# Kernel optimization log

Measured on AMD Instinct MI355X. Metric: run time of the kernel, lower is better.

## Reference

```python
import jax, jax.numpy as jnp
import numpy as np

N, B, PG, L, HC, EC, H, NC, KNN = 256, 4, 64, 32, 128, 64, 4, 14, 8
D = HC // H
CUTOFF = 10.0
LOG2 = 0.6931471805599453

_counts = np.array([14, 5, 11, 8, 8, 6, 9, 9, 4, 10, 8, 8, 9, 8, 11, 7, 6, 7, 14, 12, 7])
RES_ATOM_MASK = (np.arange(14)[None, :] < _counts[:, None]).astype(np.float32)  # [21,14]


def _ln(x, g, b):
    mu = jnp.mean(x, -1, keepdims=True)
    var = jnp.mean((x - mu) ** 2, -1, keepdims=True)
    return (x - mu) / jnp.sqrt(var + 1e-5) * g + b


def _ssp(x):
    return jax.nn.softplus(x) - LOG2


def _safe_norm(x):
    return jnp.sqrt(jnp.maximum(jnp.sum(x * x, -1), 1e-12))


def _seg_softmax(x, idx, n):
    m = jax.ops.segment_max(x, idx, num_segments=n)
    e = jnp.exp(x - m[idx])
    s = jax.ops.segment_sum(e, idx, num_segments=n)
    return e / s[idx]


def _smear(d):
    offs = jnp.linspace(0.0, CUTOFF, EC)
    coeff = -0.5 / (offs[1] - offs[0]) ** 2
    return jnp.exp(coeff * (d[..., None] - offs) ** 2)


def _core(res_H, res_X, ligand_pos, ligand_feat, ligand_mask,
          ln_g, ln_b, ln1_g, ln1_b,
          WQ, WK, WV, WKl, WVl, WO, WOl, WOl1,
          Ti_w1, Ti_b1, Ti_w2, Ti_b2,
          sD_w1, sD_b1, sD_w2, sD_b2,
          sD1_w1, sD1_b1, sD1_w2, sD1_b2,
          res_S, batch, residue_mask, row1, col1):
    n = res_H.shape[0]
    bsz = ligand_feat.shape[0]
    lc = ligand_feat.shape[1]
    amask = jnp.asarray(RES_ATOM_MASK)[res_S]  # [n,14]

    # kNN graph on C-alpha (atom 1), per-graph, flow target_to_source, + self loops
    ctr = res_X[:, 1]
    d2 = jnp.sum((ctr[:, None] - ctr[None]) ** 2, -1)
    bad = (batch[:, None] != batch[None]) | jnp.eye(n, dtype=bool)
    _, nbr = jax.lax.top_k(-jnp.where(bad, jnp.inf, d2), KNN)
    row = jnp.concatenate([jnp.repeat(jnp.arange(n), KNN), jnp.arange(n)])
    col = jnp.concatenate([nbr.reshape(-1), jnp.arange(n)])

    Rij = _safe_norm(res_X[row][:, :, None] - res_X[col][:, None])  # [E,14,14]
    drep = _smear(Rij)  # [E,14,14,EC]

    res_Hn = _ln(res_H, ln_g, ln_b)
    Q = (res_Hn @ WQ.T).reshape(n, NC, H, D)
    Kt = (res_Hn @ WK.T).reshape(n, NC, H, D)
    V = (res_Hn @ WV.T).reshape(n, NC, H, D)

    logits = jnp.einsum('ephd,eqhd->ehpq', Q[row], Kt[col]) / np.sqrt(D)
    sig = jax.nn.relu(drep @ sD_w1.T + sD_b1) @ sD_w2.T + sD_b2  # [E,14,14,H]
    logits = logits + sig.transpose(0, 3, 1, 2)

    am_e = amask[row][:, :, None] * amask[col][:, None]  # [E,14,14]
    r = jnp.einsum('ep,ehpq,eq->eh', amask[row], logits, amask[col])
    r = r / jnp.sum(am_e, (-1, -2))[:, None]
    beta = _seg_softmax(r, row, n)  # [E,H]

    att = jax.nn.softmax(logits, -1) * am_e[:, None]
    att = att / (jnp.sum(jnp.abs(att), -1, keepdims=True) + 1e-7)
    aV = jnp.einsum('ehpq,eqhd->ehpd', att, V[col])
    updH = jax.ops.segment_sum(beta[:, :, None, None] * aV, row, num_segments=n)
    updH = updH.transpose(0, 2, 1, 3).reshape(n, NC, HC)
    res_H2 = (res_Hn + _ssp(updH) @ WO.T) * amask[..., None]

    Xij = res_X[row][:, :, None] - res_X[col][:, None]  # [E,14,14,3]
    Xij = Xij / (_safe_norm(Xij)[..., None] + 1e-5)
    Qf = Q.reshape(n, NC, HC)
    Kf = Kt.reshape(n, NC, HC)
    # T_i on concat([Q_p, K_q, dist]) computed as split matmuls (no big concat)
    hmid = (Qf[row] @ Ti_w1[:, :HC].T)[:, :, None, :] \
        + (Kf[col] @ Ti_w1[:, HC:2 * HC].T)[:, None, :, :] \
        + drep @ Ti_w1[:, 2 * HC:].T + Ti_b1  # [E,14,14,HC]
    f = (jax.nn.relu(hmid) @ Ti_w2.T + Ti_b2)[..., 0]  # [E,14,14]
    f = f * jnp.mean(att, 1)
    dX = jax.ops.segment_sum(jnp.mean(beta, -1)[:, None, None]
                             * jnp.sum(f[..., None] * Xij, -2), row, num_segments=n)
    res_X2 = jnp.where(residue_mask[:, None, None],
                       res_X + jnp.clip(dX, -3.0, 3.0), res_X)

    # residue <-> ligand cross attention over (editable residue, graph) edges
    lf = _ln(ligand_feat, ln1_g, ln1_b)
    Kl = (lf @ WKl.T).reshape(bsz, lc, H, D)
    Vl = (lf @ WVl.T).reshape(bsz, lc, H, D)
    Rij1 = _safe_norm(res_X2[row1][:, :, None] - ligand_pos[col1][:, None])
    drep1 = _smear(Rij1)  # [E1,14,L,EC]
    lg = jnp.einsum('ephd,eqhd->ehpq', Q[row1], Kl[col1]) / np.sqrt(D)
    sig1 = jax.nn.relu(drep1 @ sD1_w1.T + sD1_b1) @ sD1_w2.T + sD1_b2
    lg = lg + sig1.transpose(0, 3, 1, 2)

    am1 = amask[row1][:, :, None] * ligand_mask[col1][:, None]  # [E1,14,L]
    r1 = jnp.einsum('ep,ehpq,eq->eh', amask[row1], lg, ligand_mask[col1])
    r1 = r1 / jnp.sum(am1, (-1, -2))[:, None]
    beta1 = _seg_softmax(r1, col1, bsz)

    ar = jax.nn.softmax(lg, -1) * am1[:, None]
    ar = ar / (jnp.sum(jnp.abs(ar), -1, keepdims=True) + 1e-7)
    al = jax.nn.softmax(lg, -2) * am1[:, None]
    # faithful to source: lig branch divided by L1 norm of already-normalized ar
    al = al / (jnp.sum(jnp.abs(ar), -1, keepdims=True) + 1e-7)
    aVr = jnp.einsum('ehpq,eqhd->ehpd', ar, Vl[col1])  # [E1,H,14,D]
    e1 = row1.shape[0]
    res_H3 = res_H2.at[row1].add(
        _ssp(aVr.transpose(0, 2, 1, 3).reshape(e1, NC, HC)) @ WOl.T)
    res_H3 = res_H3 * amask[..., None]
    aVlg = jnp.einsum('ehpq,ephd->ehqd', al, V[row1])  # [E1,H,L,D]
    updL = jax.ops.segment_sum(beta1[:, :, None, None] * aVlg, col1, num_segments=bsz)
    lf2 = lf + _ssp(updL.transpose(0, 2, 1, 3).reshape(bsz, lc, HC)) @ WOl1.T
    return res_H3, res_X2, lf2


def setup_inputs() -> dict:
    key = jax.random.key(0)
    ks = jax.random.split(key, 40)
    rn = lambda i, shape, s=1.0: jax.random.normal(ks[i], shape, jnp.float32) * s
    w = lambda i, shape: jax.random.normal(ks[i], shape, jnp.float32) * 0.05
    res_H = rn(0, (N, NC, HC))
    res_X = rn(1, (N, NC, 3), 4.0)
    res_S = jax.random.randint(ks[2], (N,), 0, 21)
    batch = jnp.repeat(jnp.arange(B), PG)
    residue_mask = (jnp.arange(N) % PG) < 16
    row1 = jnp.asarray(np.nonzero(np.asarray(residue_mask))[0])
    col1 = row1 // PG
    ligand_pos = rn(3, (B, L, 3), 4.0)
    ligand_feat = rn(4, (B, L, HC))
    ligand_mask = jnp.tile((jnp.arange(L) < 24).astype(jnp.float32)[None], (B, 1))
    return dict(
        res_H=res_H, res_X=res_X, ligand_pos=ligand_pos, ligand_feat=ligand_feat,
        ligand_mask=ligand_mask,
        ln_g=jnp.ones((HC,)), ln_b=jnp.zeros((HC,)),
        ln1_g=jnp.ones((HC,)), ln1_b=jnp.zeros((HC,)),
        WQ=w(5, (HC, HC)), WK=w(6, (HC, HC)), WV=w(7, (HC, HC)),
        WKl=w(8, (HC, HC)), WVl=w(9, (HC, HC)),
        WO=w(10, (HC, HC)), WOl=w(11, (HC, HC)), WOl1=w(12, (HC, HC)),
        Ti_w1=w(13, (HC, 2 * HC + EC)), Ti_b1=jnp.zeros((HC,)),
        Ti_w2=w(14, (1, HC)), Ti_b2=jnp.zeros((1,)),
        sD_w1=w(15, (HC, EC)), sD_b1=jnp.zeros((HC,)),
        sD_w2=w(16, (H, HC)), sD_b2=jnp.zeros((H,)),
        sD1_w1=w(17, (HC, EC)), sD1_b1=jnp.zeros((HC,)),
        sD1_w2=w(18, (H, HC)), sD1_b2=jnp.zeros((H,)),
        res_S=res_S, batch=batch, residue_mask=residue_mask, row1=row1, col1=col1)


def reference(res_H, res_X, ligand_pos, ligand_feat, ligand_mask,
              ln_g, ln_b, ln1_g, ln1_b,
              WQ, WK, WV, WKl, WVl, WO, WOl, WOl1,
              Ti_w1, Ti_b1, Ti_w2, Ti_b2,
              sD_w1, sD_b1, sD_w2, sD_b2,
              sD1_w1, sD1_b1, sD1_w2, sD1_b2,
              res_S, batch, residue_mask, row1, col1):
    return _core(res_H, res_X, ligand_pos, ligand_feat, ligand_mask,
                 ln_g, ln_b, ln1_g, ln1_b,
                 WQ, WK, WV, WKl, WVl, WO, WOl, WOl1,
                 Ti_w1, Ti_b1, Ti_w2, Ti_b2,
                 sD_w1, sD_b1, sD_w2, sD_b2,
                 sD1_w1, sD1_b1, sD1_w2, sD1_b2,
                 res_S, batch, residue_mask, row1, col1)
```

## Files before the change

### kernel.cpp

```cpp
#include <hip/hip_runtime.h>
#include <hip/hip_bf16.h>
#include <math.h>

typedef __hip_bfloat16 bf16;

#define NRES 256
#define LC   32
#define HCH  128
#define ECH  64
#define NH   4
#define NCA  14
#define KNNK 8
#define DH   32
#define NKE  (NRES*KNNK)
#define NEDGE (NKE+NRES)
#define NE1  64
#define NROWS (NRES*NCA)

#define NT     3073
#define TSCALE 256.0f
#define DMAXT  12.0f

#define O_RESH   0
#define O_RESX   458752
#define O_LPOS   469504
#define O_LFEAT  469888
#define O_LMASK  486272
#define O_LNG    486400
#define O_LNB    486528
#define O_LN1G   486656
#define O_LN1B   486784
#define O_WQ     486912
#define O_WK     503296
#define O_WV     519680
#define O_WKL    536064
#define O_WVL    552448
#define O_WO     568832
#define O_WOL    585216
#define O_WOL1   601600
#define O_TIW1   617984
#define O_TIB1   658944
#define O_TIW2   659072
#define O_TIB2   659200
#define O_SDW1   659204
#define O_SDB1   667396
#define O_SDW2   667524
#define O_SDB2   668036
#define O_SD1W1  668040
#define O_SD1B1  676232
#define O_SD1W2  676360
#define O_SD1B2  676872
#define TOTCVT   676876
#define CVT_RSV  676880

#define OUTX_OFF 458752
#define OUTL_OFF 469504

__constant__ int c_counts[21] = {14,5,11,8,8,6,9,9,4,10,8,8,9,8,11,7,6,7,14,12,7};

__device__ __forceinline__ float b2f(bf16 x){ return __bfloat162float(x); }
__device__ __forceinline__ float sspf(float x){
  return fmaxf(x,0.f) + log1pf(expf(-fabsf(x))) - 0.6931471805599453f;
}
__device__ __forceinline__ float bflo(unsigned u){ return __uint_as_float(u<<16); }
__device__ __forceinline__ float bfhi(unsigned u){ return __uint_as_float(u & 0xffff0000u); }
__device__ __forceinline__ unsigned short f2bs(float v){ bf16 b=__float2bfloat16(v); return *(unsigned short*)&b; }
__device__ __forceinline__ unsigned pack2(float a, float b){
  return (unsigned)f2bs(a) | ((unsigned)f2bs(b)<<16);
}
__device__ __forceinline__ int ccount(int s){ return c_counts[s<0?0:(s>20?20:s)]; }
__device__ __forceinline__ void storeOut(void* out, int isbf, int idx, float v){
  if (isbf) ((bf16*)out)[idx] = __float2bfloat16(v);
  else      ((float*)out)[idx] = v;
}

__global__ __launch_bounds__(256) void kcvt(
    const void* s0,const void* s1,const void* s2,const void* s3,const void* s4,
    const void* s5,const void* s6,const void* s7,const void* s8,const void* s9,
    const void* s10,const void* s11,const void* s12,const void* s13,const void* s14,
    const void* s15,const void* s16,const void* s17,const void* s18,const void* s19,
    const void* s20,const void* s21,const void* s22,const void* s23,const void* s24,
    const void* s25,const void* s26,const void* s27,const void* s28,
    float* __restrict__ dst, int* __restrict__ flag)
{
  __shared__ int sflag;
  int tid = threadIdx.x;
  if (tid < 64){
    unsigned w = ((const unsigned*)s0)[tid];
    unsigned lo = w & 0xFFFFu;
    int ee = (lo >> 7) & 0xFF;
    int good = (lo == 0u) || (ee >= 121 && ee <= 133);
    unsigned long long m = __ballot(good);
    if (tid == 0){
      sflag = (__popcll(m) >= 40) ? 1 : 0;
      if (blockIdx.x == 0) flag[0] = sflag;
    }
  }
  __syncthreads();
  int isbf = sflag;
  int g = blockIdx.x*256 + tid;
  if (g >= TOTCVT) return;
  const void* src; int l;
  if      (g < O_RESX ) { src=s0;  l=g; }
  else if (g < O_LPOS ) { src=s1;  l=g-O_RESX; }
  else if (g < O_LFEAT) { src=s2;  l=g-O_LPOS; }
  else if (g < O_LMASK) { src=s3;  l=g-O_LFEAT; }
  else if (g < O_LNG  ) { src=s4;  l=g-O_LMASK; }
  else if (g < O_LNB  ) { src=s5;  l=g-O_LNG; }
  else if (g < O_LN1G ) { src=s6;  l=g-O_LNB; }
  else if (g < O_LN1B ) { src=s7;  l=g-O_LN1G; }
  else if (g < O_WQ   ) { src=s8;  l=g-O_LN1B; }
  else if (g < O_WK   ) { src=s9;  l=g-O_WQ; }
  else if (g < O_WV   ) { src=s10; l=g-O_WK; }
  else if (g < O_WKL  ) { src=s11; l=g-O_WV; }
  else if (g < O_WVL  ) { src=s12; l=g-O_WKL; }
  else if (g < O_WO   ) { src=s13; l=g-O_WVL; }
  else if (g < O_WOL  ) { src=s14; l=g-O_WO; }
  else if (g < O_WOL1 ) { src=s15; l=g-O_WOL; }
  else if (g < O_TIW1 ) { src=s16; l=g-O_WOL1; }
  else if (g < O_TIB1 ) { src=s17; l=g-O_TIW1; }
  else if (g < O_TIW2 ) { src=s18; l=g-O_TIB1; }
  else if (g < O_TIB2 ) { src=s19; l=g-O_TIW2; }
  else if (g < O_SDW1 ) { src=s20; l=0; }
  else if (g < O_SDB1 ) { src=s21; l=g-O_SDW1; }
  else if (g < O_SDW2 ) { src=s22; l=g-O_SDB1; }
  else if (g < O_SDB2 ) { src=s23; l=g-O_SDW2; }
  else if (g < O_SD1W1) { src=s24; l=g-O_SDB2; }
  else if (g < O_SD1B1) { src=s25; l=g-O_SD1W1; }
  else if (g < O_SD1W2) { src=s26; l=g-O_SD1B1; }
  else if (g < O_SD1B2) { src=s27; l=g-O_SD1W2; }
  else                  { src=s28; l=g-O_SD1B2; }
  float v = isbf ? b2f(((const bf16*)src)[l]) : ((const float*)src)[l];
  dst[g] = v;
}

__global__ __launch_bounds__(128) void kprep(const float* __restrict__ cvt, const int* __restrict__ row1,
    float* __restrict__ cT, float* __restrict__ sigT, float* __restrict__ sig1T,
    float* __restrict__ wt, int* __restrict__ inv_row)
{
  int b = blockIdx.x, o = threadIdx.x;
  if (b >= NT){
    int cb = b - NT;
    if (cb < 1280){
      int gid = cb*128 + o;
      int m = gid >> 14;
      int j = gid & 16383;
      int oo = j >> 7, c = j & 127;
      float v;
      switch(m){
        case 0: v = cvt[O_WQ  + j]; break;
        case 1: v = cvt[O_WK  + j]; break;
        case 2: v = cvt[O_WV  + j]; break;
        case 3: v = cvt[O_WO  + j]; break;
        case 4: v = cvt[O_WKL + j]; break;
        case 5: v = cvt[O_WVL + j]; break;
        case 6: v = cvt[O_WOL + j]; break;
        case 7: v = cvt[O_WOL1+ j]; break;
        case 8: v = cvt[O_TIW1 + oo*320 + c]; break;
        default:v = cvt[O_TIW1 + oo*320 + 128 + c]; break;
      }
      wt[m*16384 + c*128 + oo] = v;
    } else {
      for (int i=o;i<NRES;i+=128) inv_row[i] = -1;
      __syncthreads();
      if (o < NE1) inv_row[row1[o] & 255] = o;
    }
    return;
  }
  __shared__ float dr[64];
  __shared__ float W[128*65];
  __shared__ float h1[128], h1b[128];
  float d = (float)b * (1.0f/256.0f);
  const float step = 10.0f/63.0f;
  const float coef = -0.5f/(step*step);
  if (o < 64){ float t = d - step*(float)o; dr[o] = expf(coef*t*t); }
  for (int idx=o; idx<8192; idx+=128){ int oo=idx>>6, k=idx&63; W[oo*65+k] = cvt[O_TIW1 + oo*320 + 256 + k]; }
  __syncthreads();
  {
    float c = cvt[O_TIB1+o];
    for (int k=0;k<64;k++) c += dr[k]*W[o*65+k];
    cT[b*128+o] = c;
  }
  __syncthreads();
  for (int idx=o; idx<8192; idx+=128){ int oo=idx>>6, k=idx&63; W[oo*65+k] = cvt[O_SDW1 + idx]; }
  __syncthreads();
  {
    float a = cvt[O_SDB1+o];
    for (int k=0;k<64;k++) a += dr[k]*W[o*65+k];
    h1[o] = fmaxf(a,0.f);
  }
  __syncthreads();
  for (int idx=o; idx<8192; idx+=128){ int oo=idx>>6, k=idx&63; W[oo*65+k] = cvt[O_SD1W1 + idx]; }
  __syncthreads();
  {
    float a2 = cvt[O_SD1B1+o];
    for (int k=0;k<64;k++) a2 += dr[k]*W[o*65+k];
    h1b[o] = fmaxf(a2,0.f);
  }
  __syncthreads();
  if (o < 8){
    int h = o & 3;
    const float* hh = (o<4)? h1 : h1b;
    int wbase = (o<4)? O_SDW2 : O_SD1W2;
    int bbase = (o<4)? O_SDB2 : O_SD1B2;
    float s = cvt[bbase + h];
    for (int k=0;k<128;k++) s += hh[k]*cvt[wbase + h*128 + k];
    if (o<4) sigT[b*4+h] = s; else sig1T[b*4+h] = s;
  }
}

__global__ __launch_bounds__(256) void kProjAll(
    const float* __restrict__ cvt, const float* __restrict__ wt, const int* __restrict__ batch,
    float* __restrict__ resHn, bf16* __restrict__ Qw16, bf16* __restrict__ Kw16,
    bf16* __restrict__ Vw16, bf16* __restrict__ TQw16, bf16* __restrict__ TKw16,
    int* __restrict__ nbr, float* __restrict__ lf, bf16* __restrict__ Klw16, bf16* __restrict__ Vlw16)
{
  __shared__ float Xs[16*129];
  __shared__ float x2[2][HCH];
  __shared__ float sred2[2][2];
  int bb = blockIdx.x, tid = threadIdx.x;

  if (bb < 672){
    int m = bb / 224;
    int rt = (bb % 224) * 16;
    for (int i=tid; i<16*128; i+=256){
      int r=i>>7, c=i&127;
      Xs[r*129+c] = cvt[O_RESH + (rt+r)*HCH + c];
    }
    __syncthreads();
    {
      int wave = tid>>6, lane = tid&63;
      int r = wave*4 + (lane>>4);
      int cb = lane & 15;
      float s=0;
      #pragma unroll
      for (int j=0;j<8;j++) s += Xs[r*129 + cb + 16*j];
      #pragma unroll
      for (int off=1; off<16; off<<=1) s += __shfl_xor(s, off);
      float mu = s*(1.f/HCH);
      float q=0;
      #pragma unroll
      for (int j=0;j<8;j++){ float dv = Xs[r*129+cb+16*j]-mu; q += dv*dv; }
      #pragma unroll
      for (int off=1; off<16; off<<=1) q += __shfl_xor(q, off);
      float inv = rsqrtf(q*(1.f/HCH) + 1e-5f);
      #pragma unroll
      for (int j=0;j<8;j++){
        int c = cb + 16*j;
        float xh = (Xs[r*129+c]-mu)*inv*cvt[O_LNG+c] + cvt[O_LNB+c];
        Xs[r*129+c] = xh;
        if (m==0) resHn[(rt+r)*HCH+c] = xh;
      }
    }
    __syncthreads();
    int tc = (tid & 31) * 4;
    int tr = (tid >> 5) * 2;
    const float* W = wt + m*16384;
    float a00=0,a01=0,a02=0,a03=0, a10=0,a11=0,a12=0,a13=0;
    for (int c=0;c<HCH;c++){
      float4 w4 = *(const float4*)(W + c*128 + tc);
      float x0 = Xs[tr*129 + c];
      float x1 = Xs[(tr+1)*129 + c];
      a00 += x0*w4.x; a01 += x0*w4.y; a02 += x0*w4.z; a03 += x0*w4.w;
      a10 += x1*w4.x; a11 += x1*w4.y; a12 += x1*w4.z; a13 += x1*w4.w;
    }
    bf16* out = (m==0)? Qw16 : (m==1)? Kw16 : Vw16;
    {
      unsigned* o0 = (unsigned*)(out + (rt+tr  )*HCH + tc);
      unsigned* o1 = (unsigned*)(out + (rt+tr+1)*HCH + tc);
      o0[0]=pack2(a00,a01); o0[1]=pack2(a02,a03);
      o1[0]=pack2(a10,a11); o1[1]=pack2(a12,a13);
    }
    if (m == 2) return;
    __syncthreads();
    Xs[tr*129+tc]=a00; Xs[tr*129+tc+1]=a01; Xs[tr*129+tc+2]=a02; Xs[tr*129+tc+3]=a03;
    Xs[(tr+1)*129+tc]=a10; Xs[(tr+1)*129+tc+1]=a11; Xs[(tr+1)*129+tc+2]=a12; Xs[(tr+1)*129+tc+3]=a13;
    __syncthreads();
    const float* W2 = wt + (8+m)*16384;
    a00=0;a01=0;a02=0;a03=0; a10=0;a11=0;a12=0;a13=0;
    for (int c=0;c<HCH;c++){
      float4 w4 = *(const float4*)(W2 + c*128 + tc);
      float x0 = Xs[tr*129 + c];
      float x1 = Xs[(tr+1)*129 + c];
      a00 += x0*w4.x; a01 += x0*w4.y; a02 += x0*w4.z; a03 += x0*w4.w;
      a10 += x1*w4.x; a11 += x1*w4.y; a12 += x1*w4.z; a13 += x1*w4.w;
    }
    bf16* out2 = m ? TKw16 : TQw16;
    {
      unsigned* o0 = (unsigned*)(out2 + (rt+tr  )*HCH + tc);
      unsigned* o1 = (unsigned*)(out2 + (rt+tr+1)*HCH + tc);
      o0[0]=pack2(a00,a01); o0[1]=pack2(a02,a03);
      o1[0]=pack2(a10,a11); o1[1]=pack2(a12,a13);
    }
    return;
  }

  if (bb < 736){
    int wave = tid>>6, lane = tid&63;
    int n = (bb-672)*4 + wave;
    float cx = cvt[O_RESX+(n*NCA+1)*3+0];
    float cy = cvt[O_RESX+(n*NCA+1)*3+1];
    float cz = cvt[O_RESX+(n*NCA+1)*3+2];
    int bn = batch[n];
    float d2v[4]; int idv[4];
    #pragma unroll
    for (int t=0;t<4;t++){
      int j = lane + 64*t;
      float jx = cvt[O_RESX+(j*NCA+1)*3+0];
      float jy = cvt[O_RESX+(j*NCA+1)*3+1];
      float jz = cvt[O_RESX+(j*NCA+1)*3+2];
      float dx=cx-jx, dy=cy-jy, dz=cz-jz;
      float d2 = dx*dx+dy*dy+dz*dz;
      bool bad = (batch[j]!=bn) || (j==n);
      d2v[t] = bad ? INFINITY : d2;
      idv[t] = j;
    }
    for (int k=0;k<KNNK;k++){
      float dm = d2v[0]; int im = idv[0];
      #pragma unroll
      for (int t=1;t<4;t++)
        if (d2v[t]<dm || (d2v[t]==dm && idv[t]<im)){ dm=d2v[t]; im=idv[t]; }
      #pragma unroll
      for (int off=1; off<64; off<<=1){
        float dn = __shfl_xor(dm, off);
        int   in = __shfl_xor(im, off);
        if (dn<dm || (dn==dm && in<im)){ dm=dn; im=in; }
      }
      if (lane==0) nbr[n*KNNK+k] = im;
      #pragma unroll
      for (int t=0;t<4;t++) if (idv[t]==im) d2v[t] = INFINITY;
    }
    return;
  }

  int row = tid>>7, t = tid&127;
  int rb = (bb-736)*2 + row;
  float v = cvt[O_LFEAT + rb*HCH + t];
  float s=v;
  for (int off=1; off<64; off<<=1) s += __shfl_xor(s, off);
  if ((t&63)==0) sred2[row][t>>6]=s;
  __syncthreads();
  float mu=(sred2[row][0]+sred2[row][1])*(1.f/HCH);
  __syncthreads();
  float d=v-mu; s=d*d;
  for (int off=1; off<64; off<<=1) s += __shfl_xor(s, off);
  if ((t&63)==0) sred2[row][t>>6]=s;
  __syncthreads();
  float var=(sred2[row][0]+sred2[row][1])*(1.f/HCH);
  float xh = d*rsqrtf(var+1e-5f)*cvt[O_LN1G+t] + cvt[O_LN1B+t];
  x2[row][t]=xh; lf[rb*HCH+t]=xh;
  __syncthreads();
  const float* WKlt = wt + 4*16384;
  const float* WVlt = wt + 5*16384;
  float aK=0.f, aV=0.f;
  for (int c=0;c<HCH;c++){
    float xc=x2[row][c];
    aK += xc*WKlt[c*128+t];
    aV += xc*WVlt[c*128+t];
  }
  Klw16[rb*HCH+t]=__float2bfloat16(aK);
  Vlw16[rb*HCH+t]=__float2bfloat16(aV);
}

__global__ __launch_bounds__(256) void k3_edge(
    const float* __restrict__ cvt, const int* __restrict__ res_S, const int* __restrict__ nbr,
    const bf16* __restrict__ Qw16, const bf16* __restrict__ Kw16,
    const bf16* __restrict__ TQw16, const bf16* __restrict__ TKw16,
    const bf16* __restrict__ Vw16, const float* __restrict__ cT, const float* __restrict__ sigT,
    float* __restrict__ r_ws, bf16* __restrict__ aVe16, float* __restrict__ dXe)
{
  __shared__ unsigned Bq[14*66], Bk[14*66], Tq[14*66], Tk[14*66];
  __shared__ float LG[784], FR[196];
  __shared__ float tw2s[128], tb2s[1], Xr[42], Xc[42], amr[14], amc[14], rpart[56], cnts[2];
  unsigned* Vc = Tq;

  int b = blockIdx.x, tid = threadIdx.x;
  int rr = b & 255, slot = b >> 8;
  int e  = (slot < 8) ? (rr*8 + slot) : (2048 + rr);
  int cc = (slot < 8) ? (nbr[rr*8 + slot] & 255) : rr;

  const unsigned* Q32  = (const unsigned*)Qw16;
  const unsigned* K32  = (const unsigned*)Kw16;
  const unsigned* TQ32 = (const unsigned*)TQw16;
  const unsigned* TK32 = (const unsigned*)TKw16;
  const unsigned* V32  = (const unsigned*)Vw16;

  for (int i=tid;i<NCA*64;i+=256){
    int p=i>>6, k=i&63;
    Bq[p*66+k]=Q32[rr*896+i];  Bk[p*66+k]=K32[cc*896+i];
    Tq[p*66+k]=TQ32[rr*896+i]; Tk[p*66+k]=TK32[cc*896+i];
  }
  if (tid < 128) tw2s[tid]=cvt[O_TIW2+tid];
  if (tid == 128) tb2s[0]=cvt[O_TIB2];
  if (tid >= 136 && tid < 178){
    int i=tid-136; int p=i/3, jx=i%3;
    Xr[i] = cvt[O_RESX+(rr*NCA+p)*3+jx];
    Xc[i] = cvt[O_RESX+(cc*NCA+p)*3+jx];
  }
  if (tid >= 242 && tid < 242+NCA){
    int p=tid-242;
    amr[p] = (p < ccount(res_S[rr])) ? 1.f : 0.f;
    amc[p] = (p < ccount(res_S[cc])) ? 1.f : 0.f;
  }
  __syncthreads();

  if (tid < 196){
    int p = tid/14, q = tid%14;
    float dx=Xr[p*3]-Xc[q*3], dy=Xr[p*3+1]-Xc[q*3+1], dz=Xr[p*3+2]-Xc[q*3+2];
    float d = sqrtf(fmaxf(dx*dx+dy*dy+dz*dz, 1e-12f));
    int i0 = (int)(fminf(d, DMAXT)*TSCALE + 0.5f);
    float4 sg = ((const float4*)sigT)[i0];
    const float4* crow = (const float4*)(cT + i0*128);
    const uint2* Tq2 = (const uint2*)Tq;
    const uint2* Tk2 = (const uint2*)Tk;
    const uint2* Bq2 = (const uint2*)Bq;
    const uint2* Bk2 = (const uint2*)Bk;
    float fa = tb2s[0];
    #pragma unroll 8
    for (int j=0;j<32;j++){
      float4 cb = crow[j];
      uint2 ta = Tq2[p*33 + j];
      uint2 ka = Tk2[q*33 + j];
      int o = 4*j;
      fa += fmaxf(bflo(ta.x)+bflo(ka.x)+cb.x, 0.f)*tw2s[o  ];
      fa += fmaxf(bfhi(ta.x)+bfhi(ka.x)+cb.y, 0.f)*tw2s[o+1];
      fa += fmaxf(bflo(ta.y)+bflo(ka.y)+cb.z, 0.f)*tw2s[o+2];
      fa += fmaxf(bfhi(ta.y)+bfhi(ka.y)+cb.w, 0.f)*tw2s[o+3];
    }
    float qk0=0,qk1=0,qk2=0,qk3=0;
    #pragma unroll
    for (int j=0;j<8;j++){
      uint2 a0=Bq2[p*33+j],    b0=Bk2[q*33+j];
      uint2 a1=Bq2[p*33+8+j],  b1=Bk2[q*33+8+j];
      uint2 a2=Bq2[p*33+16+j], b2=Bk2[q*33+16+j];
      uint2 a3=Bq2[p*33+24+j], b3=Bk2[q*33+24+j];
      qk0 += bflo(a0.x)*bflo(b0.x) + bfhi(a0.x)*bfhi(b0.x) + bflo(a0.y)*bflo(b0.y) + bfhi(a0.y)*bfhi(b0.y);
      qk1 += bflo(a1.x)*bflo(b1.x) + bfhi(a1.x)*bfhi(b1.x) + bflo(a1.y)*bflo(b1.y) + bfhi(a1.y)*bfhi(b1.y);
      qk2 += bflo(a2.x)*bflo(b2.x) + bfhi(a2.x)*bfhi(b2.x) + bflo(a2.y)*bflo(b2.y) + bfhi(a2.y)*bfhi(b2.y);
      qk3 += bflo(a3.x)*bflo(b3.x) + bfhi(a3.x)*bfhi(b3.x) + bflo(a3.y)*bflo(b3.y) + bfhi(a3.y)*bfhi(b3.y);
    }
    const float isq = 0.17677669529663687f;
    LG[0*196+tid] = qk0*isq + sg.x;
    LG[1*196+tid] = qk1*isq + sg.y;
    LG[2*196+tid] = qk2*isq + sg.z;
    LG[3*196+tid] = qk3*isq + sg.w;
    FR[tid] = fa;
  }
  __syncthreads();

  for (int i=tid;i<NCA*64;i+=256){
    int p=i>>6, k=i&63;
    Vc[p*66+k]=V32[cc*896+i];
  }
  if (tid < 56){
    int h=tid/14, pp=tid%14;
    float ap = amr[pp];
    float row[NCA];
    float s=0;
    #pragma unroll
    for (int qq=0;qq<NCA;qq++){ row[qq]=LG[h*196+pp*14+qq]; s += row[qq]*amc[qq]; }
    rpart[h*14+pp] = s*ap;
    float m=-INFINITY;
    #pragma unroll
    for (int qq=0;qq<NCA;qq++) m=fmaxf(m,row[qq]);
    float sum=0;
    #pragma unroll
    for (int qq=0;qq<NCA;qq++){ row[qq]=expf(row[qq]-m); sum+=row[qq]; }
    float inv=1.f/sum, s2=0;
    #pragma unroll
    for (int qq=0;qq<NCA;qq++){ row[qq]=row[qq]*inv*ap*amc[qq]; s2+=row[qq]; }
    float inv2=1.f/(s2+1e-7f);
    #pragma unroll
    for (int qq=0;qq<NCA;qq++) LG[h*196+pp*14+qq]=row[qq]*inv2;
  }
  if (tid == 56){
    float sr=0, sc=0;
    for (int i=0;i<NCA;i++){ sr+=amr[i]; sc+=amc[i]; }
    cnts[0]=sr; cnts[1]=sc;
  }
  __syncthreads();
  if (tid < NH){
    float s=0;
    for (int pp=0;pp<NCA;pp++) s += rpart[tid*14+pp];
    r_ws[e*NH+tid] = s/(cnts[0]*cnts[1]);
  }
  if (tid < 196){
    int p=tid/14, q=tid%14;
    float ma = 0.25f*(LG[p*14+q] + LG[196+p*14+q] + LG[392+p*14+q] + LG[588+p*14+q]);
    FR[tid] *= ma;
  }
  __syncthreads();
  if (tid < NCA){
    int pp=tid;
    float ax=0, ay=0, az=0;
    #pragma unroll
    for (int qq=0;qq<NCA;qq++){
      float dx=Xr[pp*3]-Xc[qq*3], dy=Xr[pp*3+1]-Xc[qq*3+1], dz=Xr[pp*3+2]-Xc[qq*3+2];
      float nrm = sqrtf(fmaxf(dx*dx+dy*dy+dz*dz,1e-12f));
      float sc = FR[pp*14+qq]/(nrm+1e-5f);
      ax += sc*dx; ay += sc*dy; az += sc*dz;
    }
    dXe[(e*NCA+pp)*3+0]=ax; dXe[(e*NCA+pp)*3+1]=ay; dXe[(e*NCA+pp)*3+2]=az;
  }
  unsigned* aVe32 = (unsigned*)aVe16;
  #pragma unroll
  for (int rep=0;rep<4;rep++){
    int jdx = rep*256 + tid;
    if (jdx < 896){
      int h = jdx/224, rem = jdx%224;
      int pp = rem>>4, ddp = rem&15;
      float a0=0, a1=0;
      #pragma unroll
      for (int qq=0;qq<NCA;qq++){
        unsigned v = Vc[qq*66 + h*16 + ddp];
        float l = LG[h*196+pp*14+qq];
        a0 += l*bflo(v);
        a1 += l*bfhi(v);
      }
      aVe32[e*896 + jdx] = pack2(a0,a1);
    }
  }
}

__global__ __launch_bounds__(256) void k4_agg(
    const float* __restrict__ cvt, const int* __restrict__ res_S, const int* __restrict__ inv_row,
    const float* __restrict__ r_ws, const bf16* __restrict__ aVe16, const float* __restrict__ dXe,
    const float* __restrict__ resHn, const float* __restrict__ wt, const int* __restrict__ flag,
    float* __restrict__ resH2, float* __restrict__ resX2, void* __restrict__ d_out)
{
  int n = blockIdx.x, tid = threadIdx.x;
  __shared__ float beta[9][NH];
  __shared__ float betam[9];
  __shared__ float Xs[NCA][HCH];
  if (tid < NH){
    int h = tid;
    float rv[9], m=-INFINITY;
    #pragma unroll
    for (int k=0;k<9;k++){
      int ek = (k<KNNK)? n*KNNK+k : NKE+n;
      rv[k] = r_ws[ek*NH+h];
      m = fmaxf(m, rv[k]);
    }
    float s=0;
    #pragma unroll
    for (int k=0;k<9;k++){ rv[k]=expf(rv[k]-m); s+=rv[k]; }
    #pragma unroll
    for (int k=0;k<9;k++) beta[k][h]=rv[k]/s;
  }
  __syncthreads();
  if (tid < 9) betam[tid] = 0.25f*(beta[tid][0]+beta[tid][1]+beta[tid][2]+beta[tid][3]);
  int col = tid & 127, ph = tid >> 7;
  int h = col>>5, dd = col&31;
  float bh[9];
  #pragma unroll
  for (int k=0;k<9;k++) bh[k]=beta[k][h];
  #pragma unroll
  for (int i=0;i<7;i++){
    int p = ph + 2*i;
    float u=0;
    #pragma unroll
    for (int k=0;k<9;k++){
      int ek = (k<KNNK)? n*KNNK+k : NKE+n;
      u += bh[k]*b2f(aVe16[ek*1792 + h*448 + p*32 + dd]);
    }
    Xs[p][col] = sspf(u);
  }
  __syncthreads();
  const float* WOt = wt + 3*16384;
  float acc[7];
  #pragma unroll
  for (int i=0;i<7;i++) acc[i]=0.f;
  for (int c=0;c<HCH;c++){
    float w = WOt[c*128+col];
    #pragma unroll
    for (int i=0;i<7;i++) acc[i] += Xs[ph+2*i][c]*w;
  }
  int cnt = ccount(res_S[n]);
  #pragma unroll
  for (int i=0;i<7;i++){
    int p = ph + 2*i;
    float am = (p<cnt)?1.f:0.f;
    float outv = (resHn[(n*NCA+p)*HCH+col] + acc[i])*am;
    resH2[(n*NCA+p)*HCH+col] = outv;
  }
  if (tid < NCA*3){
    int isbf = *flag;
    int p=tid/3, jx=tid%3;
    float s=0;
    #pragma unroll
    for (int k=0;k<9;k++){
      int ek=(k<KNNK)? n*KNNK+k : NKE+n;
      s += betam[k]*dXe[(ek*NCA+p)*3+jx];
    }
    float base = cvt[O_RESX+(n*NCA+p)*3+jx];
    float v = (inv_row[n]>=0) ? base + fminf(fmaxf(s,-3.f),3.f) : base;
    resX2[(n*NCA+p)*3+jx] = v;
    storeOut(d_out, isbf, OUTX_OFF + (n*NCA+p)*3+jx, v);
  }
}

__global__ __launch_bounds__(256) void k6_lig(
    const float* __restrict__ cvt, const int* __restrict__ res_S,
    const int* __restrict__ row1, const int* __restrict__ col1,
    const float* __restrict__ resX2, const bf16* __restrict__ Qw16, const bf16* __restrict__ Klw16,
    const bf16* __restrict__ Vw16, const bf16* __restrict__ Vlw16, const float* __restrict__ sig1T,
    float* __restrict__ r1_ws, float* __restrict__ aVr, float* __restrict__ aVlg)
{
  __shared__ __align__(16) float S[10042];
  float* Bq  = S;
  float* Bk  = S + 1848;
  float* LG  = S;
  float* Vl  = S + 1848;
  float* ALs = S + 6104;
  float* Vr  = S + 7896;
  float* EX  = S + 9744;
  float* Xr = EX;
  float* Lp = EX + 42;
  float* amr = EX + 138;
  float* lm  = EX + 152;
  float* s2r = EX + 184;
  float* rpart = EX + 240;
  float* cnts  = EX + 296;
  int e = blockIdx.x, tid = threadIdx.x;
  int rr = row1[e] & 255, cb = col1[e] & 3;

  for (int i=tid;i<NCA*HCH;i+=256){ int p=i>>7,c=i&127; Bq[p*132+c]=b2f(Qw16[rr*1792+i]); Vr[p*132+c]=b2f(Vw16[rr*1792+i]); }
  for (int i=tid;i<LC*HCH;i+=256){ int q=i>>7,c=i&127; Bk[q*133+c]=b2f(Klw16[cb*LC*HCH+i]); }
  if (tid >= 8 && tid < 50){ int i=tid-8; int p=i/3,jx=i%3; Xr[i]=resX2[(rr*NCA+p)*3+jx]; }
  if (tid >= 64 && tid < 160){ int i=tid-64; int q=i/3,jx=i%3; Lp[i]=cvt[O_LPOS+(cb*LC+q)*3+jx]; }
  if (tid >= 160 && tid < 160+NCA) amr[tid-160]=((tid-160) < ccount(res_S[rr]))?1.f:0.f;
  if (tid >= 192 && tid < 224) lm[tid-192]=cvt[O_LMASK + cb*LC + tid-192];
  __syncthreads();

  float l0[2][4];
  int npair = (tid < 192) ? 2 : 1;
  for (int w=0; w<npair; w++){
    int pair = tid + w*256;
    int p = pair>>5, q = pair&31;
    float dx=Xr[p*3]-Lp[q*3], dy=Xr[p*3+1]-Lp[q*3+1], dz=Xr[p*3+2]-Lp[q*3+2];
    float d = sqrtf(fmaxf(dx*dx+dy*dy+dz*dz,1e-12f));
    int i0 = (int)(fminf(d, DMAXT)*TSCALE + 0.5f);
    float4 sg = ((const float4*)sig1T)[i0];
    float q0=0,q1=0,q2=0,q3=0;
    #pragma unroll
    for (int dd=0;dd<DH;dd++){
      q0 += Bq[p*132+dd]   *Bk[q*133+dd];
      q1 += Bq[p*132+32+dd]*Bk[q*133+32+dd];
      q2 += Bq[p*132+64+dd]*Bk[q*133+64+dd];
      q3 += Bq[p*132+96+dd]*Bk[q*133+96+dd];
    }
    const float isq=0.17677669529663687f;
    l0[w][0]=q0*isq+sg.x; l0[w][1]=q1*isq+sg.y; l0[w][2]=q2*isq+sg.z; l0[w][3]=q3*isq+sg.w;
  }
  __syncthreads();
  for (int w=0; w<npair; w++){
    int pair = tid + w*256;
    LG[0*448+pair]=l0[w][0]; LG[1*448+pair]=l0[w][1]; LG[2*448+pair]=l0[w][2]; LG[3*448+pair]=l0[w][3];
  }
  for (int i=tid;i<LC*HCH;i+=256){ int q=i>>7,c=i&127; Vl[q*132+c]=b2f(Vlw16[cb*LC*HCH+i]); }
  __syncthreads();

  if (tid < 56){
    int h=tid/14, pp=tid%14;
    float ap=amr[pp];
    float s=0, m=-INFINITY;
    for (int qq=0;qq<LC;qq++){ float v=LG[h*448+pp*32+qq]; s+=v*lm[qq]; m=fmaxf(m,v); }
    rpart[h*14+pp]=s*ap;
    float sum=0;
    for (int qq=0;qq<LC;qq++) sum+=expf(LG[h*448+pp*32+qq]-m);
    float inv=1.f/sum, s2=0;
    for (int qq=0;qq<LC;qq++) s2 += expf(LG[h*448+pp*32+qq]-m)*inv*ap*lm[qq];
    s2r[h*14+pp] = s2/(s2+1e-7f);
  }
  if (tid==56){
    float sr=0,sl=0;
    for(int i=0;i<NCA;i++) sr+=amr[i];
    for(int i=0;i<LC;i++) sl+=lm[i];
    cnts[0]=sr; cnts[1]=sl;
  }
  __syncthreads();
  if (tid < NH){
    float s=0; for (int pp=0;pp<NCA;pp++) s+=rpart[tid*14+pp];
    r1_ws[e*NH+tid]=s/(cnts[0]*cnts[1]);
  }
  if (tid < NH*LC){
    int h=tid>>5, qq=tid&31;
    float m=-INFINITY;
    for (int pp=0;pp<NCA;pp++) m=fmaxf(m,LG[h*448+pp*32+qq]);
    float sum=0;
    for (int pp=0;pp<NCA;pp++) sum+=expf(LG[h*448+pp*32+qq]-m);
    float inv=1.f/sum;
    float lq=lm[qq];
    for (int pp=0;pp<NCA;pp++){
      float a=expf(LG[h*448+pp*32+qq]-m)*inv*amr[pp]*lq;
      ALs[h*448+pp*32+qq]=a/(s2r[h*14+pp]+1e-7f);
    }
  }
  __syncthreads();
  if (tid < 56){
    int h=tid/14, pp=tid%14;
    float ap=amr[pp];
    float m=-INFINITY;
    for (int qq=0;qq<LC;qq++) m=fmaxf(m,LG[h*448+pp*32+qq]);
    float row[LC];
    float sum=0;
    for (int qq=0;qq<LC;qq++){ row[qq]=expf(LG[h*448+pp*32+qq]-m); sum+=row[qq]; }
    float inv=1.f/sum, s2=0;
    for (int qq=0;qq<LC;qq++){ row[qq]=row[qq]*inv*ap*lm[qq]; s2+=row[qq]; }
    float inv2=1.f/(s2+1e-7f);
    for (int qq=0;qq<LC;qq++) LG[h*448+pp*32+qq]=row[qq]*inv2;
  }
  __syncthreads();
  for (int j=tid;j<NH*NCA*DH;j+=256){
    int h=j/448, rem=j%448, pp=rem>>5, dd=rem&31;
    float acc=0;
    #pragma unroll
    for (int qq=0;qq<LC;qq++) acc += LG[h*448+pp*32+qq]*Vl[qq*132+h*32+dd];
    aVr[e*1792+j]=acc;
  }
  for (int j=tid;j<NH*LC*DH;j+=256){
    int h=j>>10, rem=j&1023, qq=rem>>5, dd=rem&31;
    float acc=0;
    #pragma unroll
    for (int pp=0;pp<NCA;pp++) acc += ALs[h*448+pp*32+qq]*Vr[pp*132+h*32+dd];
    aVlg[e*4096+j]=acc;
  }
}

__global__ __launch_bounds__(256) void k78_final(
    const int* __restrict__ inv_row, const int* __restrict__ res_S, const int* __restrict__ col1,
    const float* __restrict__ resH2, const float* __restrict__ aVr,
    const float* __restrict__ r1_ws, const float* __restrict__ aVlg, const float* __restrict__ lf,
    const float* __restrict__ wt, const int* __restrict__ flag, void* __restrict__ d_out)
{
  int bb = blockIdx.x, tid = threadIdx.x;
  if (bb < 256){
    int n = bb;
    int e = inv_row[n];
    __shared__ float G[NCA][HCH];
    if (e>=0){
      for (int j=tid;j<NCA*HCH;j+=256){
        int h=j/448, rem=j%448, pp=rem>>5, dd=rem&31;
        G[pp][h*DH+dd] = sspf(aVr[e*1792+j]);
      }
    }
    __syncthreads();
    int col = tid & 127, ph = tid >> 7;
    float acc[7];
    #pragma unroll
    for (int i=0;i<7;i++) acc[i]=0.f;
    if (e>=0){
      const float* WOlt = wt + 6*16384;
      for (int c=0;c<HCH;c++){
        float w=WOlt[c*128+col];
        #pragma unroll
        for (int i=0;i<7;i++) acc[i]+=G[ph+2*i][c]*w;
      }
    }
    int cnt=ccount(res_S[n]);
    int isbf = *flag;
    #pragma unroll
    for (int i=0;i<7;i++){
      int p = ph + 2*i;
      float am=(p<cnt)?1.f:0.f;
      float v=(resH2[(n*NCA+p)*HCH+col]+acc[i])*am;
      storeOut(d_out, isbf, (n*NCA+p)*HCH+col, v);
    }
    return;
  }
  int rb = bb - 256;
  int b = rb>>5, q = rb&31;
  __shared__ float bw[NE1][NH];
  __shared__ float xs[HCH];
  if (tid<NH){
    int h=tid;
    float m=-INFINITY;
    for (int e=0;e<NE1;e++) if ((col1[e]&3)==b) m=fmaxf(m, r1_ws[e*NH+h]);
    float s=0;
    for (int e=0;e<NE1;e++) if ((col1[e]&3)==b) s+=expf(r1_ws[e*NH+h]-m);
    for (int e=0;e<NE1;e++) bw[e][h] = ((col1[e]&3)==b)? expf(r1_ws[e*NH+h]-m)/s : 0.f;
  }
  __syncthreads();
  if (tid < 128){
    int h=tid>>5, dd=tid&31;
    float u=0;
    for (int e=0;e<NE1;e++) u += bw[e][h]*aVlg[e*4096 + h*1024 + q*32 + dd];
    xs[tid]=sspf(u);
  }
  __syncthreads();
  if (tid < 128){
    const float* WOl1t = wt + 7*16384;
    float acc=0;
    for (int c=0;c<HCH;c++) acc += xs[c]*WOl1t[c*128+tid];
    float v = lf[rb*HCH+tid] + acc;
    storeOut(d_out, *flag, OUTL_OFF + rb*HCH+tid, v);
  }
}

extern "C" void kernel_launch(void* const* d_in, const int* in_sizes, int n_in,
                              void* d_out, int out_size, void* d_ws, size_t ws_size,
                              hipStream_t stream)
{
  const int* res_S = (const int*)d_in[29];
  const int* batch = (const int*)d_in[30];
  const int* row1  = (const int*)d_in[32];
  const int* col1  = (const int*)d_in[33];

  float* wsf = (float*)d_ws;
  size_t o = 0;
  int*   flag    = (int*)(wsf + o); o += 4;
  float* cvt     = wsf + o; o += CVT_RSV;
  float* wt      = wsf + o; o += 10*16384;
  int*   inv_row = (int*)(wsf + o); o += 256;
  int*   nbr     = (int*)(wsf + o); o += NRES*KNNK;
  float* resHn   = wsf + o; o += NROWS*HCH;
  bf16*  Qw16    = (bf16*)(wsf + o); o += NROWS*HCH/2;
  bf16*  Kw16    = (bf16*)(wsf + o); o += NROWS*HCH/2;
  bf16*  Vw16    = (bf16*)(wsf + o); o += NROWS*HCH/2;
  bf16*  TQw16   = (bf16*)(wsf + o); o += NROWS*HCH/2;
  bf16*  TKw16   = (bf16*)(wsf + o); o += NROWS*HCH/2;
  float* r_ws    = wsf + o; o += NEDGE*NH;
  bf16*  aVe16   = (bf16*)(wsf + o); o += (size_t)NEDGE*1792/2;
  float* dXe     = wsf + o; o += NEDGE*NCA*3;
  float* resH2   = wsf + o; o += NROWS*HCH;
  float* resX2   = wsf + o; o += NRES*NCA*3;
  float* lf      = wsf + o; o += 4*LC*HCH;
  bf16*  Klw16   = (bf16*)(wsf + o); o += 4*LC*HCH/2;
  bf16*  Vlw16   = (bf16*)(wsf + o); o += 4*LC*HCH/2;
  float* r1w     = wsf + o; o += NE1*NH;
  float* aVrw    = wsf + o; o += NE1*1792;
  float* aVlgw   = wsf + o; o += NE1*4096;
  float* cT      = wsf + o; o += (size_t)NT*128;
  float* sigT    = wsf + o; o += NT*4;
  float* sig1T   = wsf + o; o += NT*4;

  kcvt<<<(TOTCVT+255)/256, 256, 0, stream>>>(
      d_in[0],d_in[1],d_in[2],d_in[3],d_in[4],d_in[5],d_in[6],d_in[7],d_in[8],
      d_in[9],d_in[10],d_in[11],d_in[12],d_in[13],d_in[14],d_in[15],d_in[16],
      d_in[17],d_in[18],d_in[19],d_in[20],d_in[21],d_in[22],d_in[23],d_in[24],
      d_in[25],d_in[26],d_in[27],d_in[28], cvt, flag);
  kprep<<<NT + 1280 + 1, 128, 0, stream>>>(cvt, row1, cT, sigT, sig1T, wt, inv_row);
  kProjAll<<<800, 256, 0, stream>>>(cvt, wt, batch, resHn, Qw16, Kw16, Vw16, TQw16, TKw16,
                                    nbr, lf, Klw16, Vlw16);
  k3_edge<<<NEDGE, 256, 0, stream>>>(cvt, res_S, nbr, Qw16, Kw16, TQw16, TKw16, Vw16, cT, sigT,
                                     r_ws, aVe16, dXe);
  k4_agg<<<NRES, 256, 0, stream>>>(cvt, res_S, inv_row, r_ws, aVe16, dXe, resHn, wt, flag,
                                   resH2, resX2, d_out);
  k6_lig<<<NE1, 256, 0, stream>>>(cvt, res_S, row1, col1, resX2, Qw16, Klw16, Vw16, Vlw16, sig1T,
                                  r1w, aVrw, aVlgw);
  k78_final<<<384, 256, 0, stream>>>(inv_row, res_S, col1, resH2, aVrw, r1w, aVlgw, lf,
                                     wt, flag, d_out);
}
```

Before: 279.3 us.

## Fuse weight transpose into convert kernel, batch table build, widen edge LDS loads

```diff
diff --git a/kernel.cpp b/kernel.cpp
--- a/kernel.cpp
+++ b/kernel.cpp
@@ -52,9 +52,12 @@
 #define O_SD1B2  676872
 #define TOTCVT   676876
 #define CVT_RSV  676880
+#define NCVTB    2645
 
 #define OUTX_OFF 458752
 #define OUTL_OFF 469504
+
+#define SR3 68
 
 __constant__ int c_counts[21] = {14,5,11,8,8,6,9,9,4,10,8,8,9,8,11,7,6,7,14,12,7};
 
@@ -81,10 +84,18 @@
     const void* s15,const void* s16,const void* s17,const void* s18,const void* s19,
     const void* s20,const void* s21,const void* s22,const void* s23,const void* s24,
     const void* s25,const void* s26,const void* s27,const void* s28,
-    float* __restrict__ dst, int* __restrict__ flag)
+    const int* __restrict__ row1,
+    float* __restrict__ dst, float* __restrict__ wt, int* __restrict__ inv_row,
+    int* __restrict__ flag)
 {
+  int tid = threadIdx.x;
+  if (blockIdx.x == NCVTB){
+    if (tid < NRES) inv_row[tid] = -1;
+    __syncthreads();
+    if (tid < NE1) inv_row[row1[tid] & 255] = tid;
+    return;
+  }
   __shared__ int sflag;
-  int tid = threadIdx.x;
   if (tid < 64){
     unsigned w = ((const unsigned*)s0)[tid];
     unsigned lo = w & 0xFFFFu;
@@ -132,80 +143,79 @@
   else                  { src=s28; l=g-O_SD1B2; }
   float v = isbf ? b2f(((const bf16*)src)[l]) : ((const float*)src)[l];
   dst[g] = v;
-}
-
-__global__ __launch_bounds__(128) void kprep(const float* __restrict__ cvt, const int* __restrict__ row1,
-    float* __restrict__ cT, float* __restrict__ sigT, float* __restrict__ sig1T,
-    float* __restrict__ wt, int* __restrict__ inv_row)
+  if (g >= O_WQ && g < O_TIW1){
+    int r = (g-O_WQ)>>14, j = (g-O_WQ)&16383;
+    int oo = j>>7, c = j&127;
+    int slot = (r==3)?4 : (r==4)?5 : (r==5)?3 : r;
+    wt[slot*16384 + c*128 + oo] = v;
+  } else if (g >= O_TIW1 && g < O_TIB1){
+    int ll = g - O_TIW1;
+    int oo = ll/320, c = ll - oo*320;
+    if (c < 128)      wt[8*16384 + c*128 + oo] = v;
+    else if (c < 256) wt[9*16384 + (c-128)*128 + oo] = v;
+  }
+}
+
+__global__ __launch_bounds__(128) void ktab(const float* __restrict__ cvt,
+    float* __restrict__ cT, float* __restrict__ sigT, float* __restrict__ sig1T)
 {
   int b = blockIdx.x, o = threadIdx.x;
-  if (b >= NT){
-    int cb = b - NT;
-    if (cb < 1280){
-      int gid = cb*128 + o;
-      int m = gid >> 14;
-      int j = gid & 16383;
-      int oo = j >> 7, c = j & 127;
-      float v;
-      switch(m){
-        case 0: v = cvt[O_WQ  + j]; break;
-        case 1: v = cvt[O_WK  + j]; break;
-        case 2: v = cvt[O_WV  + j]; break;
-        case 3: v = cvt[O_WO  + j]; break;
-        case 4: v = cvt[O_WKL + j]; break;
-        case 5: v = cvt[O_WVL + j]; break;
-        case 6: v = cvt[O_WOL + j]; break;
-        case 7: v = cvt[O_WOL1+ j]; break;
-        case 8: v = cvt[O_TIW1 + oo*320 + c]; break;
-        default:v = cvt[O_TIW1 + oo*320 + 128 + c]; break;
-      }
-      wt[m*16384 + c*128 + oo] = v;
-    } else {
-      for (int i=o;i<NRES;i+=128) inv_row[i] = -1;
-      __syncthreads();
-      if (o < NE1) inv_row[row1[o] & 255] = o;
-    }
-    return;
-  }
-  __shared__ float dr[64];
+  int i0 = b*16;
   __shared__ float W[128*65];
-  __shared__ float h1[128], h1b[128];
-  float d = (float)b * (1.0f/256.0f);
+  __shared__ float dr[16][65];
+  __shared__ float h1[16][130];
+  __shared__ float h1b[16][130];
   const float step = 10.0f/63.0f;
   const float coef = -0.5f/(step*step);
-  if (o < 64){ float t = d - step*(float)o; dr[o] = expf(coef*t*t); }
+  for (int idx=o; idx<16*64; idx+=128){
+    int i=idx>>6, k=idx&63;
+    float d = (float)(i0+i)*(1.0f/256.0f);
+    float t = d - step*(float)k;
+    dr[i][k] = expf(coef*t*t);
+  }
   for (int idx=o; idx<8192; idx+=128){ int oo=idx>>6, k=idx&63; W[oo*65+k] = cvt[O_TIW1 + oo*320 + 256 + k]; }
   __syncthreads();
   {
-    float c = cvt[O_TIB1+o];
-    for (int k=0;k<64;k++) c += dr[k]*W[o*65+k];
-    cT[b*128+o] = c;
+    float bias = cvt[O_TIB1+o];
+    for (int i=0;i<16 && i0+i<NT;i++){
+      float c = bias;
+      for (int k=0;k<64;k++) c += dr[i][k]*W[o*65+k];
+      cT[(i0+i)*128+o] = c;
+    }
   }
   __syncthreads();
   for (int idx=o; idx<8192; idx+=128){ int oo=idx>>6, k=idx&63; W[oo*65+k] = cvt[O_SDW1 + idx]; }
   __syncthreads();
   {
-    float a = cvt[O_SDB1+o];
-    for (int k=0;k<64;k++) a += dr[k]*W[o*65+k];
-    h1[o] = fmaxf(a,0.f);
+    float bias = cvt[O_SDB1+o];
+    for (int i=0;i<16;i++){
+      float a = bias;
+      for (int k=0;k<64;k++) a += dr[i][k]*W[o*65+k];
+      h1[i][o] = fmaxf(a,0.f);
+    }
   }
   __syncthreads();
   for (int idx=o; idx<8192; idx+=128){ int oo=idx>>6, k=idx&63; W[oo*65+k] = cvt[O_SD1W1 + idx]; }
   __syncthreads();
   {
-    float a2 = cvt[O_SD1B1+o];
-    for (int k=0;k<64;k++) a2 += dr[k]*W[o*65+k];
-    h1b[o] = fmaxf(a2,0.f);
-  }
-  __syncthreads();
-  if (o < 8){
-    int h = o & 3;
-    const float* hh = (o<4)? h1 : h1b;
-    int wbase = (o<4)? O_SDW2 : O_SD1W2;
-    int bbase = (o<4)? O_SDB2 : O_SD1B2;
-    float s = cvt[bbase + h];
-    for (int k=0;k<128;k++) s += hh[k]*cvt[wbase + h*128 + k];
-    if (o<4) sigT[b*4+h] = s; else sig1T[b*4+h] = s;
+    float bias = cvt[O_SD1B1+o];
+    for (int i=0;i<16;i++){
+      float a = bias;
+      for (int k=0;k<64;k++) a += dr[i][k]*W[o*65+k];
+      h1b[i][o] = fmaxf(a,0.f);
+    }
+  }
+  __syncthreads();
+  {
+    int i = o>>3, sub = o&7, h = sub&3, path = sub>>2;
+    if (i0+i < NT){
+      const float* hh = path ? h1b[i] : h1[i];
+      int wbase = path ? O_SD1W2 : O_SDW2;
+      int bbase = path ? O_SD1B2 : O_SDB2;
+      float s = cvt[bbase + h];
+      for (int k=0;k<128;k++) s += hh[k]*cvt[wbase + h*128 + k];
+      if (path) sig1T[(i0+i)*4+h] = s; else sigT[(i0+i)*4+h] = s;
+    }
   }
 }
 
@@ -369,7 +379,7 @@
     const bf16* __restrict__ Vw16, const float* __restrict__ cT, const float* __restrict__ sigT,
     float* __restrict__ r_ws, bf16* __restrict__ aVe16, float* __restrict__ dXe)
 {
-  __shared__ unsigned Bq[14*66], Bk[14*66], Tq[14*66], Tk[14*66];
+  __shared__ __align__(16) unsigned Bq[14*SR3], Bk[14*SR3], Tq[14*SR3], Tk[14*SR3];
   __shared__ float LG[784], FR[196];
   __shared__ float tw2s[128], tb2s[1], Xr[42], Xc[42], amr[14], amc[14], rpart[56], cnts[2];
   unsigned* Vc = Tq;
@@ -387,8 +397,8 @@
 
   for (int i=tid;i<NCA*64;i+=256){
     int p=i>>6, k=i&63;
-    Bq[p*66+k]=Q32[rr*896+i];  Bk[p*66+k]=K32[cc*896+i];
-    Tq[p*66+k]=TQ32[rr*896+i]; Tk[p*66+k]=TK32[cc*896+i];
+    Bq[p*SR3+k]=Q32[rr*896+i];  Bk[p*SR3+k]=K32[cc*896+i];
+    Tq[p*SR3+k]=TQ32[rr*896+i]; Tk[p*SR3+k]=TK32[cc*896+i];
   }
   if (tid < 128) tw2s[tid]=cvt[O_TIW2+tid];
   if (tid == 128) tb2s[0]=cvt[O_TIB2];
@@ -411,33 +421,41 @@
     int i0 = (int)(fminf(d, DMAXT)*TSCALE + 0.5f);
     float4 sg = ((const float4*)sigT)[i0];
     const float4* crow = (const float4*)(cT + i0*128);
-    const uint2* Tq2 = (const uint2*)Tq;
-    const uint2* Tk2 = (const uint2*)Tk;
-    const uint2* Bq2 = (const uint2*)Bq;
-    const uint2* Bk2 = (const uint2*)Bk;
+    const uint4* Tq4 = (const uint4*)Tq;
+    const uint4* Tk4 = (const uint4*)Tk;
+    const uint4* Bq4 = (const uint4*)Bq;
+    const uint4* Bk4 = (const uint4*)Bk;
     float fa = tb2s[0];
-    #pragma unroll 8
-    for (int j=0;j<32;j++){
-      float4 cb = crow[j];
-      uint2 ta = Tq2[p*33 + j];
-      uint2 ka = Tk2[q*33 + j];
-      int o = 4*j;
-      fa += fmaxf(bflo(ta.x)+bflo(ka.x)+cb.x, 0.f)*tw2s[o  ];
-      fa += fmaxf(bfhi(ta.x)+bfhi(ka.x)+cb.y, 0.f)*tw2s[o+1];
-      fa += fmaxf(bflo(ta.y)+bflo(ka.y)+cb.z, 0.f)*tw2s[o+2];
-      fa += fmaxf(bfhi(ta.y)+bfhi(ka.y)+cb.w, 0.f)*tw2s[o+3];
+    #pragma unroll 4
+    for (int j=0;j<16;j++){
+      uint4 ta = Tq4[p*17 + j];
+      uint4 ka = Tk4[q*17 + j];
+      float4 cb0 = crow[2*j], cb1 = crow[2*j+1];
+      int o = 8*j;
+      fa += fmaxf(bflo(ta.x)+bflo(ka.x)+cb0.x, 0.f)*tw2s[o  ];
+      fa += fmaxf(bfhi(ta.x)+bfhi(ka.x)+cb0.y, 0.f)*tw2s[o+1];
+      fa += fmaxf(bflo(ta.y)+bflo(ka.y)+cb0.z, 0.f)*tw2s[o+2];
+      fa += fmaxf(bfhi(ta.y)+bfhi(ka.y)+cb0.w, 0.f)*tw2s[o+3];
+      fa += fmaxf(bflo(ta.z)+bflo(ka.z)+cb1.x, 0.f)*tw2s[o+4];
+      fa += fmaxf(bfhi(ta.z)+bfhi(ka.z)+cb1.y, 0.f)*tw2s[o+5];
+      fa += fmaxf(bflo(ta.w)+bflo(ka.w)+cb1.z, 0.f)*tw2s[o+6];
+      fa += fmaxf(bfhi(ta.w)+bfhi(ka.w)+cb1.w, 0.f)*tw2s[o+7];
     }
     float qk0=0,qk1=0,qk2=0,qk3=0;
     #pragma unroll
-    for (int j=0;j<8;j++){
-      uint2 a0=Bq2[p*33+j],    b0=Bk2[q*33+j];
-      uint2 a1=Bq2[p*33+8+j],  b1=Bk2[q*33+8+j];
-      uint2 a2=Bq2[p*33+16+j], b2=Bk2[q*33+16+j];
-      uint2 a3=Bq2[p*33+24+j], b3=Bk2[q*33+24+j];
-      qk0 += bflo(a0.x)*bflo(b0.x) + bfhi(a0.x)*bfhi(b0.x) + bflo(a0.y)*bflo(b0.y) + bfhi(a0.y)*bfhi(b0.y);
-      qk1 += bflo(a1.x)*bflo(b1.x) + bfhi(a1.x)*bfhi(b1.x) + bflo(a1.y)*bflo(b1.y) + bfhi(a1.y)*bfhi(b1.y);
-      qk2 += bflo(a2.x)*bflo(b2.x) + bfhi(a2.x)*bfhi(b2.x) + bflo(a2.y)*bflo(b2.y) + bfhi(a2.y)*bfhi(b2.y);
-      qk3 += bflo(a3.x)*bflo(b3.x) + bfhi(a3.x)*bfhi(b3.x) + bflo(a3.y)*bflo(b3.y) + bfhi(a3.y)*bfhi(b3.y);
+    for (int j=0;j<4;j++){
+      uint4 a0=Bq4[p*17+j],    b0=Bk4[q*17+j];
+      uint4 a1=Bq4[p*17+4+j],  b1=Bk4[q*17+4+j];
+      uint4 a2=Bq4[p*17+8+j],  b2=Bk4[q*17+8+j];
+      uint4 a3=Bq4[p*17+12+j], b3=Bk4[q*17+12+j];
+      qk0 += bflo(a0.x)*bflo(b0.x) + bfhi(a0.x)*bfhi(b0.x) + bflo(a0.y)*bflo(b0.y) + bfhi(a0.y)*bfhi(b0.y)
+           + bflo(a0.z)*bflo(b0.z) + bfhi(a0.z)*bfhi(b0.z) + bflo(a0.w)*bflo(b0.w) + bfhi(a0.w)*bfhi(b0.w);
+      qk1 += bflo(a1.x)*bflo(b1.x) + bfhi(a1.x)*bfhi(b1.x) + bflo(a1.y)*bflo(b1.y) + bfhi(a1.y)*bfhi(b1.y)
+           + bflo(a1.z)*bflo(b1.z) + bfhi(a1.z)*bfhi(b1.z) + bflo(a1.w)*bflo(b1.w) + bfhi(a1.w)*bfhi(b1.w);
+      qk2 += bflo(a2.x)*bflo(b2.x) + bfhi(a2.x)*bfhi(b2.x) + bflo(a2.y)*bflo(b2.y) + bfhi(a2.y)*bfhi(b2.y)
+           + bflo(a2.z)*bflo(b2.z) + bfhi(a2.z)*bfhi(b2.z) + bflo(a2.w)*bflo(b2.w) + bfhi(a2.w)*bfhi(b2.w);
+      qk3 += bflo(a3.x)*bflo(b3.x) + bfhi(a3.x)*bfhi(b3.x) + bflo(a3.y)*bflo(b3.y) + bfhi(a3.y)*bfhi(b3.y)
+           + bflo(a3.z)*bflo(b3.z) + bfhi(a3.z)*bfhi(b3.z) + bflo(a3.w)*bflo(b3.w) + bfhi(a3.w)*bfhi(b3.w);
     }
     const float isq = 0.17677669529663687f;
     LG[0*196+tid] = qk0*isq + sg.x;
@@ -450,7 +468,7 @@
 
   for (int i=tid;i<NCA*64;i+=256){
     int p=i>>6, k=i&63;
-    Vc[p*66+k]=V32[cc*896+i];
+    Vc[p*SR3+k]=V32[cc*896+i];
   }
   if (tid < 56){
     int h=tid/14, pp=tid%14;
@@ -512,7 +530,7 @@
       float a0=0, a1=0;
       #pragma unroll
       for (int qq=0;qq<NCA;qq++){
-        unsigned v = Vc[qq*66 + h*16 + ddp];
+        unsigned v = Vc[qq*SR3 + h*16 + ddp];
         float l = LG[h*196+pp*14+qq];
         a0 += l*bflo(v);
         a1 += l*bfhi(v);
@@ -834,12 +852,12 @@
   float* sigT    = wsf + o; o += NT*4;
   float* sig1T   = wsf + o; o += NT*4;
 
-  kcvt<<<(TOTCVT+255)/256, 256, 0, stream>>>(
+  kcvt<<<NCVTB+1, 256, 0, stream>>>(
       d_in[0],d_in[1],d_in[2],d_in[3],d_in[4],d_in[5],d_in[6],d_in[7],d_in[8],
       d_in[9],d_in[10],d_in[11],d_in[12],d_in[13],d_in[14],d_in[15],d_in[16],
       d_in[17],d_in[18],d_in[19],d_in[20],d_in[21],d_in[22],d_in[23],d_in[24],
-      d_in[25],d_in[26],d_in[27],d_in[28], cvt, flag);
-  kprep<<<NT + 1280 + 1, 128, 0, stream>>>(cvt, row1, cT, sigT, sig1T, wt, inv_row);
+      d_in[25],d_in[26],d_in[27],d_in[28], row1, cvt, wt, inv_row, flag);
+  ktab<<<(NT+15)/16, 128, 0, stream>>>(cvt, cT, sigT, sig1T);
   kProjAll<<<800, 256, 0, stream>>>(cvt, wt, batch, resHn, Qw16, Kw16, Vw16, TQw16, TKw16,
                                     nbr, lf, Klw16, Vlw16);
   k3_edge<<<NEDGE, 256, 0, stream>>>(cvt, res_S, nbr, Qw16, Kw16, TQw16, TKw16, Vw16, cT, sigT,
```

Result: slower. 285.2 us (+2.1%).
